# Kernel tuning notes

Measured on AMD Instinct MI355X. Metric: run time of the kernel, lower is better.

The kernel has to match this reference:

```python
import jax, jax.numpy as jnp
import numpy as np

B, T, C, H = 4, 2048, 1024, 16
D = C // H  # head dim = 64

def setup_inputs() -> dict:
    key = jax.random.key(0)
    k1, k2, k3 = jax.random.split(key, 3)
    x = jax.random.normal(k1, (B, T, C), dtype=jnp.float32)
    w_attn = jax.random.normal(k2, (C, 3 * C), dtype=jnp.float32) * 0.02
    b_attn = jnp.zeros((3 * C,), dtype=jnp.float32)
    w_proj = jax.random.normal(k3, (C, C), dtype=jnp.float32) * 0.02
    b_proj = jnp.zeros((C,), dtype=jnp.float32)
    return {"x": x, "w_attn": w_attn, "b_attn": b_attn, "w_proj": w_proj, "b_proj": b_proj}

def reference(x, w_attn, b_attn, w_proj, b_proj):
    Bx, Tx, Cx = x.shape
    qkv = x @ w_attn + b_attn  # [B, T, 3C]
    q, k, v = jnp.split(qkv, 3, axis=2)
    # [B, H, T, D]
    q = q.reshape(Bx, Tx, H, D).swapaxes(1, 2)
    k = k.reshape(Bx, Tx, H, D).swapaxes(1, 2)
    v = v.reshape(Bx, Tx, H, D).swapaxes(1, 2)
    scale = 1.0 / jnp.sqrt(jnp.asarray(D, dtype=x.dtype))
    att = jnp.einsum('bhqd,bhkd->bhqk', q, k) * scale  # [B, H, T, T]
    causal = jnp.tril(jnp.ones((Tx, Tx), dtype=bool))
    att = jnp.where(causal[None, None], att, -jnp.inf)
    att = jax.nn.softmax(att, axis=-1)
    y = jnp.einsum('bhqk,bhkd->bhqd', att, v)  # [B, H, T, D]
    y = y.swapaxes(1, 2).reshape(Bx, Tx, Cx)
    return y @ w_proj + b_proj
```

## Files before the change

### kernel.cpp

```cpp
#include <hip/hip_runtime.h>
#include <hip/hip_bf16.h>
#include <cstdint>

#define B_ 4
#define T_ 2048
#define C_ 1024
#define H_ 16
#define D_ 64

#define BM 128
#define BN 128
#define BK 64
#define NT (C_ / BK)

typedef __bf16 bf16x8 __attribute__((ext_vector_type(8)));
typedef float f32x4 __attribute__((ext_vector_type(4)));

static __device__ __forceinline__ unsigned short f2bf(float f) {
    unsigned int i = __float_as_uint(f);
    unsigned int r = (i + 0x7FFFu + ((i >> 16) & 1u)) >> 16;
    return (unsigned short)r;
}
static __device__ __forceinline__ unsigned short f2bf_hw(float f) {
    __bf16 h = (__bf16)f;
    union { __bf16 h; unsigned short u; } cv;
    cv.h = h;
    return cv.u;
}
static __device__ __forceinline__ float exp2_fast(float x) {
    float r;
    asm("v_exp_f32 %0, %1" : "=v"(r) : "v"(x));
    return r;
}

static __device__ __forceinline__ void gl_lds16(const unsigned short* g,
                                                unsigned short* l) {
    __builtin_amdgcn_global_load_lds(
        (const __attribute__((address_space(1))) unsigned int*)g,
        (__attribute__((address_space(3))) unsigned int*)l, 16, 0, 0);
}

__global__ __launch_bounds__(256)
void convert_f32_bf16(const float* __restrict__ in,
                      unsigned short* __restrict__ out, int n) {
    int i = (blockIdx.x * 256 + threadIdx.x) * 8;
    if (i < n) {
        float4 a = *(const float4*)(in + i);
        float4 b = *(const float4*)(in + i + 4);
        ushort4 s0 = {f2bf(a.x), f2bf(a.y), f2bf(a.z), f2bf(a.w)};
        ushort4 s1 = {f2bf(b.x), f2bf(b.y), f2bf(b.z), f2bf(b.w)};
        *(ushort4*)(out + i) = s0;
        *(ushort4*)(out + i + 4) = s1;
    }
}

__global__ void transpose_f32_bf16(const float* __restrict__ in,
                                   unsigned short* __restrict__ out,
                                   int R, int Cc) {
    __shared__ unsigned short tile[32][33];
    int c0 = blockIdx.x * 32;
    int r0 = blockIdx.y * 32;
    int tx = threadIdx.x, ty = threadIdx.y;
    #pragma unroll
    for (int i = ty; i < 32; i += 8)
        tile[i][tx] = f2bf(in[(size_t)(r0 + i) * Cc + c0 + tx]);
    __syncthreads();
    #pragma unroll
    for (int i = ty; i < 32; i += 8)
        out[(size_t)(c0 + i) * R + r0 + tx] = tile[tx][i];
}

#define GEMM128_CORE(APTR, ASTRIDE, BTPTR)                                    \
    int tid = threadIdx.x;                                                    \
    int nwg = gridDim.x * gridDim.y;                                          \
    int flat = blockIdx.y * gridDim.x + blockIdx.x;                           \
    int swz = (flat & 7) * (nwg >> 3) + (flat >> 3);                          \
    int bx = swz % gridDim.x;                                                 \
    int by = swz / gridDim.x;                                                 \
    int row0 = by * BM;                                                       \
    int col0 = bx * BN;                                                       \
    int wave = tid >> 6, lane = tid & 63;                                     \
    int wm = wave >> 1, wn = wave & 1;                                        \
    int m16 = lane & 15, quad = lane >> 4;                                    \
    int srow = tid >> 3;                                                      \
    int scs = ((tid & 7) ^ (srow & 7)) * 8;                                   \
    const unsigned short* aps = (APTR) + (size_t)(row0 + srow) * (ASTRIDE)    \
                                + scs;                                        \
    const unsigned short* bps = (BTPTR) + (size_t)(col0 + srow) * C_ + scs;   \
    f32x4 acc[4][4];                                                          \
    _Pragma("unroll")                                                         \
    for (int i = 0; i < 4; ++i)                                               \
    _Pragma("unroll")                                                         \
    for (int j = 0; j < 4; ++j)                                               \
        acc[i][j] = (f32x4){0.f, 0.f, 0.f, 0.f};                              \
    auto STAGE = [&](int t, int buf) {                                        \
        int koff = t * BK;                                                    \
        unsigned short* ad = smem + buf * 8192 + tid * 8;                     \
        unsigned short* bd = smem + 16384 + buf * 8192 + tid * 8;             \
        _Pragma("unroll")                                                     \
        for (int l = 0; l < 4; ++l) {                                         \
            gl_lds16(aps + (size_t)(l * 32) * (ASTRIDE) + koff, ad + l * 2048);\
            gl_lds16(bps + (size_t)(l * 32) * C_ + koff, bd + l * 2048);      \
        }                                                                     \
    };                                                                        \
    int rbA = wm * 64 + m16;                                                  \
    int rbB = wn * 64 + m16;                                                  \
    int pc0 = ((0 + quad) ^ (m16 & 7)) * 8;                                   \
    int pc1 = ((4 + quad) ^ (m16 & 7)) * 8;                                   \
    STAGE(0, 0);                                                              \
    asm volatile("s_waitcnt vmcnt(0)" ::: "memory");                          \
    __builtin_amdgcn_s_barrier();                                             \
    for (int t = 0; t < NT; ++t) {                                            \
        int buf = t & 1;                                                      \
        if (t + 1 < NT) STAGE(t + 1, buf ^ 1);                                \
        const unsigned short* Abuf = smem + buf * 8192;                       \
        const unsigned short* Bbuf = smem + 16384 + buf * 8192;               \
        bf16x8 a0[4], a1[4], b0[4], b1[4];                                    \
        _Pragma("unroll")                                                     \
        for (int i = 0; i < 4; ++i) {                                         \
            a0[i] = *(const bf16x8*)(Abuf + (rbA + i * 16) * 64 + pc0);       \
            a1[i] = *(const bf16x8*)(Abuf + (rbA + i * 16) * 64 + pc1);       \
        }                                                                     \
        _Pragma("unroll")                                                     \
        for (int j = 0; j < 4; ++j) {                                         \
            b0[j] = *(const bf16x8*)(Bbuf + (rbB + j * 16) * 64 + pc0);       \
            b1[j] = *(const bf16x8*)(Bbuf + (rbB + j * 16) * 64 + pc1);       \
        }                                                                     \
        __builtin_amdgcn_s_setprio(1);                                        \
        _Pragma("unroll")                                                     \
        for (int i = 0; i < 4; ++i)                                           \
        _Pragma("unroll")                                                     \
        for (int j = 0; j < 4; ++j) {                                         \
            acc[i][j] = __builtin_amdgcn_mfma_f32_16x16x32_bf16(              \
                a0[i], b0[j], acc[i][j], 0, 0, 0);                            \
            acc[i][j] = __builtin_amdgcn_mfma_f32_16x16x32_bf16(              \
                a1[i], b1[j], acc[i][j], 0, 0, 0);                            \
        }                                                                     \
        __builtin_amdgcn_s_setprio(0);                                        \
        asm volatile("s_waitcnt vmcnt(0)" ::: "memory");                      \
        __builtin_amdgcn_s_barrier();                                        \
    }                                                                         \
    __syncthreads();

__global__ __launch_bounds__(256, 2)
void gemm_qkv(const unsigned short* __restrict__ A,
              const unsigned short* __restrict__ Bt,
              const float* __restrict__ bias,
              unsigned short* __restrict__ qkv,
              unsigned short* __restrict__ vt,
              int M, float qscale) {
    __shared__ __align__(16) unsigned short smem[32768];
    GEMM128_CORE(A, C_, Bt)

    float bv[4];
    #pragma unroll
    for (int j = 0; j < 4; ++j)
        bv[j] = bias[col0 + wn * 64 + j * 16 + m16];

    unsigned short* wbuf = smem + wave * 2048;
    bool isV = (col0 >= 2 * C_);
    float sc = (col0 < C_) ? qscale : 1.0f;
    int b_loc = row0 >> 11;
    int trow0 = (row0 & 2047) + wm * 64;
    int head = isV ? ((col0 - 2 * C_ + wn * 64) >> 6) : 0;
    unsigned short* vtb = vt + (size_t)((b_loc * H_ + head) * 64) * T_;

    #pragma unroll
    for (int sub = 0; sub < 4; ++sub) {
        int i0 = (sub >> 1) << 1;
        int j0 = (sub & 1) << 1;
        #pragma unroll
        for (int jj = 0; jj < 2; ++jj) {
            #pragma unroll
            for (int ii = 0; ii < 2; ++ii) {
                #pragma unroll
                for (int rr = 0; rr < 4; ++rr) {
                    int rl = ii * 16 + quad * 4 + rr;
                    int cl = jj * 16 + m16;
                    unsigned short hv =
                        f2bf((acc[i0 + ii][j0 + jj][rr] + bv[j0 + jj]) * sc);
                    if (!isV) wbuf[rl * 40 + cl] = hv;
                    else      wbuf[cl * 40 + rl] = hv;
                }
            }
        }
        __builtin_amdgcn_sched_barrier(0);
        if (!isV) {
            #pragma unroll
            for (int it = 0; it < 4; ++it) {
                int rl = it * 8 + (lane >> 3);
                int cc = (lane & 7) << 2;
                uint2 v2 = *(const uint2*)&wbuf[rl * 40 + cc];
                int rowg = row0 + wm * 64 + i0 * 16 + rl;
                int colg = col0 + wn * 64 + j0 * 16 + cc;
                *(uint2*)&qkv[(size_t)rowg * (2 * C_) + colg] = v2;
            }
        } else {
            #pragma unroll
            for (int it = 0; it < 4; ++it) {
                int dsub = it * 8 + (lane >> 3);
                int tc = (lane & 7) << 2;
                uint2 v2 = *(const uint2*)&wbuf[dsub * 40 + tc];
                int d = j0 * 16 + dsub;
                int tg = trow0 + i0 * 16 + tc;
                *(uint2*)&vtb[(size_t)d * T_ + tg] = v2;
            }
        }
        __builtin_amdgcn_sched_barrier(0);
    }
}

__global__ __launch_bounds__(256, 2)
void gemm_out(const unsigned short* __restrict__ A,
              const unsigned short* __restrict__ Bt,
              const float* __restrict__ bias,
              float* __restrict__ Cmat,
              int M) {
    const int N = C_;
    __shared__ __align__(16) unsigned short smem[32768];
    GEMM128_CORE(A, (2 * C_), Bt)

    #pragma unroll
    for (int j = 0; j < 4; ++j) {
        int col = col0 + wn * 64 + j * 16 + m16;
        float bvv = bias[col];
        #pragma unroll
        for (int i = 0; i < 4; ++i) {
            int row = row0 + wm * 64 + i * 16 + quad * 4;
            #pragma unroll
            for (int rr = 0; rr < 4; ++rr)
                Cmat[(size_t)(row + rr) * N + col] = acc[i][j][rr] + bvv;
        }
    }
}

__global__ __launch_bounds__(256, 4)
void attn_mfma(unsigned short* __restrict__ qkv,
               const unsigned short* __restrict__ vt) {
    __shared__ __align__(16) unsigned short Ks[2][64][64];
    __shared__ __align__(16) unsigned short Vs[2][64][64];
    __shared__ __align__(16) unsigned short Pb[4][16][64];

    int bh = blockIdx.x;
    int b = bh >> 4, h = bh & 15;
    int qb = (T_ / 128 - 1) - blockIdx.y;
    int tid = threadIdx.x;
    int wave = tid >> 6;
    int lane = tid & 63;
    int m16 = lane & 15, quad = lane >> 4;

    const size_t rs = 2 * C_;
    unsigned short* base = qkv + (size_t)b * T_ * rs + h * 64;
    const unsigned short* kb0 = base + C_;
    const unsigned short* vtb = vt + (size_t)bh * 64 * T_;

    bf16x8 qf0[2], qf1[2];
    #pragma unroll
    for (int f = 0; f < 2; ++f) {
        int qrow = qb * 128 + wave * 32 + f * 16 + m16;
        const unsigned short* qp = base + (size_t)qrow * rs;
        qf0[f] = *(const bf16x8*)(qp + quad * 8);
        qf1[f] = *(const bf16x8*)(qp + 32 + quad * 8);
    }

    f32x4 o[2][4];
    #pragma unroll
    for (int f = 0; f < 2; ++f)
        #pragma unroll
        for (int dt = 0; dt < 4; ++dt) o[f][dt] = (f32x4){0.f, 0.f, 0.f, 0.f};
    float lrow[2][4] = {{0.f, 0.f, 0.f, 0.f}, {0.f, 0.f, 0.f, 0.f}};

    int qg0[2];
    qg0[0] = qb * 128 + wave * 32 + quad * 4;
    qg0[1] = qg0[0] + 16;

    int ntiles = 2 * qb + 2;

    int srow = tid >> 3;
    int schs = ((tid & 7) ^ (srow & 7)) * 8;
    const unsigned short* kps = kb0 + (size_t)srow * rs + schs;
    const unsigned short* vps = vtb + (size_t)srow * T_ + schs;
    unsigned short* kdst = &Ks[0][0][0] + wave * 512;
    unsigned short* vdst = &Vs[0][0][0] + wave * 512;

    auto STAGE = [&](int kt, int buf) {
        const unsigned short* ks = kps + (size_t)(kt * 64) * rs;
        const unsigned short* vs = vps + kt * 64;
        unsigned short* kd = kdst + buf * 4096;
        unsigned short* vd = vdst + buf * 4096;
        gl_lds16(ks, kd);
        gl_lds16(ks + (size_t)32 * rs, kd + 2048);
        gl_lds16(vs, vd);
        gl_lds16(vs + (size_t)32 * T_, vd + 2048);
    };

    int kpc0 = ((0 + quad) ^ (m16 & 7)) << 3;
    int kpc1 = ((4 + quad) ^ (m16 & 7)) << 3;

    STAGE(0, 0);
    asm volatile("s_waitcnt vmcnt(0)" ::: "memory");
    __builtin_amdgcn_s_barrier();

    for (int kt = 0; kt < ntiles; ++kt) {
        int cur = kt & 1;
        if (kt + 1 < ntiles) STAGE(kt + 1, cur ^ 1);

        f32x4 s[2][4];
        #pragma unroll
        for (int st = 0; st < 4; ++st) {
            bf16x8 k0 = *(const bf16x8*)&Ks[cur][st * 16 + m16][kpc0];
            bf16x8 k1 = *(const bf16x8*)&Ks[cur][st * 16 + m16][kpc1];
            __builtin_amdgcn_s_setprio(1);
            #pragma unroll
            for (int f = 0; f < 2; ++f) {
                f32x4 a = (f32x4){0.f, 0.f, 0.f, 0.f};
                a = __builtin_amdgcn_mfma_f32_16x16x32_bf16(qf0[f], k0, a, 0, 0, 0);
                a = __builtin_amdgcn_mfma_f32_16x16x32_bf16(qf1[f], k1, a, 0, 0, 0);
                s[f][st] = a;
            }
            __builtin_amdgcn_s_setprio(0);
        }

        if (kt >= 2 * qb) {
            #pragma unroll
            for (int f = 0; f < 2; ++f)
                #pragma unroll
                for (int st = 0; st < 4; ++st) {
                    int kg = kt * 64 + st * 16 + m16;
                    #pragma unroll
                    for (int r = 0; r < 4; ++r)
                        if (kg > qg0[f] + r) s[f][st][r] = -1.0e30f;
                }
        }

        #pragma unroll
        for (int f = 0; f < 2; ++f) {
            #pragma unroll
            for (int st = 0; st < 4; ++st)
                #pragma unroll
                for (int r = 0; r < 4; ++r) {
                    float p = exp2_fast(s[f][st][r]);
                    lrow[f][r] += p;
                    int row = quad * 4 + r;
                    int phys = (st * 2 + (m16 >> 3)) ^ (row & 7);
                    Pb[wave][row][phys * 8 + (m16 & 7)] = f2bf_hw(p);
                }
            __builtin_amdgcn_sched_barrier(0);

            #pragma unroll
            for (int s2 = 0; s2 < 2; ++s2) {
                int pc = ((s2 * 4 + quad) ^ (m16 & 7)) << 3;
                bf16x8 pa = *(const bf16x8*)&Pb[wave][m16][pc];
                __builtin_amdgcn_s_setprio(1);
                #pragma unroll
                for (int dt = 0; dt < 4; ++dt) {
                    bf16x8 vv = *(const bf16x8*)&Vs[cur][dt * 16 + m16][pc];
                    o[f][dt] = __builtin_amdgcn_mfma_f32_16x16x32_bf16(
                        pa, vv, o[f][dt], 0, 0, 0);
                }
                __builtin_amdgcn_s_setprio(0);
            }
            __builtin_amdgcn_sched_barrier(0);
        }

        asm volatile("s_waitcnt vmcnt(0)" ::: "memory");
        __builtin_amdgcn_s_barrier();
    }

    #pragma unroll
    for (int f = 0; f < 2; ++f) {
        float lf[4];
        #pragma unroll
        for (int r = 0; r < 4; ++r) lf[r] = lrow[f][r];
        #pragma unroll
        for (int off = 1; off <= 8; off <<= 1)
            #pragma unroll
            for (int r = 0; r < 4; ++r)
                lf[r] += __shfl_xor(lf[r], off);

        #pragma unroll
        for (int r = 0; r < 4; ++r) {
            float inv = 1.0f / lf[r];
            unsigned short* op = base + (size_t)(qg0[f] + r) * rs;
            #pragma unroll
            for (int dt = 0; dt < 4; ++dt)
                op[dt * 16 + m16] = f2bf_hw(o[f][dt][r] * inv);
        }
    }
}

extern "C" void kernel_launch(void* const* d_in, const int* in_sizes, int n_in,
                              void* d_out, int out_size, void* d_ws, size_t ws_size,
                              hipStream_t stream) {
    const float* x      = (const float*)d_in[0];
    const float* w_attn = (const float*)d_in[1];
    const float* b_attn = (const float*)d_in[2];
    const float* w_proj = (const float*)d_in[3];
    const float* b_proj = (const float*)d_in[4];
    float* out = (float*)d_out;

    unsigned short* ws = (unsigned short*)d_ws;
    unsigned short* xb       = ws;
    unsigned short* w_attn_t = xb + (size_t)B_ * T_ * C_;
    unsigned short* w_proj_t = w_attn_t + (size_t)3 * C_ * C_;
    unsigned short* qkv      = w_proj_t + (size_t)C_ * C_;

    const size_t fixed_hw = (size_t)B_ * T_ * C_ + 4 * (size_t)C_ * C_;
    const size_t per_b_hw = (size_t)T_ * 2 * C_ + (size_t)H_ * 64 * T_;
    int bstep = (ws_size >= (fixed_hw + (size_t)B_ * per_b_hw) * sizeof(unsigned short))
                ? B_ : 1;

    int nx = B_ * T_ * C_;
    convert_f32_bf16<<<nx / 2048, 256, 0, stream>>>(x, xb, nx);
    transpose_f32_bf16<<<dim3(3 * C_ / 32, C_ / 32), dim3(32, 8), 0, stream>>>(
        w_attn, w_attn_t, C_, 3 * C_);
    transpose_f32_bf16<<<dim3(C_ / 32, C_ / 32), dim3(32, 8), 0, stream>>>(
        w_proj, w_proj_t, C_, C_);

    const float QSCALE = 0.125f * 1.44269504088896341f;

    for (int b0 = 0; b0 < B_; b0 += bstep) {
        int M = bstep * T_;
        const unsigned short* xbb = xb + (size_t)b0 * T_ * C_;
        unsigned short* vt = qkv + (size_t)bstep * T_ * 2 * C_;

        gemm_qkv<<<dim3(3 * C_ / BN, M / BM), 256, 0, stream>>>(
            xbb, w_attn_t, b_attn, qkv, vt, M, QSCALE);

        attn_mfma<<<dim3(bstep * H_, T_ / 128), 256, 0, stream>>>(qkv, vt);

        gemm_out<<<dim3(C_ / BN, M / BM), 256, 0, stream>>>(
            qkv, w_proj_t, b_proj, out + (size_t)b0 * T_ * C_, M);
    }
}
```

Measured before the change: 263.2 us.

## Triple-buffer K/V tiles in attention and batch P writes across both row fragments

```diff
diff --git a/kernel.cpp b/kernel.cpp
--- a/kernel.cpp
+++ b/kernel.cpp
@@ -234,12 +234,12 @@
     }
 }
 
-__global__ __launch_bounds__(256, 4)
+__global__ __launch_bounds__(256, 2)
 void attn_mfma(unsigned short* __restrict__ qkv,
                const unsigned short* __restrict__ vt) {
-    __shared__ __align__(16) unsigned short Ks[2][64][64];
-    __shared__ __align__(16) unsigned short Vs[2][64][64];
-    __shared__ __align__(16) unsigned short Pb[4][16][64];
+    __shared__ __align__(16) unsigned short Ks[3][64][64];
+    __shared__ __align__(16) unsigned short Vs[3][64][64];
+    __shared__ __align__(16) unsigned short Pb[4][32][64];
 
     int bh = blockIdx.x;
     int b = bh >> 4, h = bh & 15;
@@ -283,33 +283,36 @@
     unsigned short* kdst = &Ks[0][0][0] + wave * 512;
     unsigned short* vdst = &Vs[0][0][0] + wave * 512;
 
-    auto STAGE = [&](int kt, int buf) {
+    auto STAGE = [&](int kt, int off) {
         const unsigned short* ks = kps + (size_t)(kt * 64) * rs;
         const unsigned short* vs = vps + kt * 64;
-        unsigned short* kd = kdst + buf * 4096;
-        unsigned short* vd = vdst + buf * 4096;
-        gl_lds16(ks, kd);
-        gl_lds16(ks + (size_t)32 * rs, kd + 2048);
-        gl_lds16(vs, vd);
-        gl_lds16(vs + (size_t)32 * T_, vd + 2048);
+        gl_lds16(ks, kdst + off);
+        gl_lds16(ks + (size_t)32 * rs, kdst + off + 2048);
+        gl_lds16(vs, vdst + off);
+        gl_lds16(vs + (size_t)32 * T_, vdst + off + 2048);
     };
 
     int kpc0 = ((0 + quad) ^ (m16 & 7)) << 3;
     int kpc1 = ((4 + quad) ^ (m16 & 7)) << 3;
 
     STAGE(0, 0);
-    asm volatile("s_waitcnt vmcnt(0)" ::: "memory");
+    STAGE(1, 4096);
+    asm volatile("s_waitcnt vmcnt(4)" ::: "memory");
     __builtin_amdgcn_s_barrier();
 
+    int o0 = 0, o1 = 4096, o2 = 8192;
     for (int kt = 0; kt < ntiles; ++kt) {
-        int cur = kt & 1;
-        if (kt + 1 < ntiles) STAGE(kt + 1, cur ^ 1);
+        bool st2 = (kt + 2 < ntiles);
+        if (st2) STAGE(kt + 2, o2);
+
+        const unsigned short* Kc = &Ks[0][0][0] + o0;
+        const unsigned short* Vc = &Vs[0][0][0] + o0;
 
         f32x4 s[2][4];
         #pragma unroll
         for (int st = 0; st < 4; ++st) {
-            bf16x8 k0 = *(const bf16x8*)&Ks[cur][st * 16 + m16][kpc0];
-            bf16x8 k1 = *(const bf16x8*)&Ks[cur][st * 16 + m16][kpc1];
+            bf16x8 k0 = *(const bf16x8*)(Kc + (st * 16 + m16) * 64 + kpc0);
+            bf16x8 k1 = *(const bf16x8*)(Kc + (st * 16 + m16) * 64 + kpc1);
             __builtin_amdgcn_s_setprio(1);
             #pragma unroll
             for (int f = 0; f < 2; ++f) {
@@ -334,37 +337,43 @@
         }
 
         #pragma unroll
-        for (int f = 0; f < 2; ++f) {
+        for (int f = 0; f < 2; ++f)
             #pragma unroll
             for (int st = 0; st < 4; ++st)
                 #pragma unroll
                 for (int r = 0; r < 4; ++r) {
                     float p = exp2_fast(s[f][st][r]);
                     lrow[f][r] += p;
-                    int row = quad * 4 + r;
+                    int row = f * 16 + quad * 4 + r;
                     int phys = (st * 2 + (m16 >> 3)) ^ (row & 7);
                     Pb[wave][row][phys * 8 + (m16 & 7)] = f2bf_hw(p);
                 }
-            __builtin_amdgcn_sched_barrier(0);
-
-            #pragma unroll
-            for (int s2 = 0; s2 < 2; ++s2) {
-                int pc = ((s2 * 4 + quad) ^ (m16 & 7)) << 3;
-                bf16x8 pa = *(const bf16x8*)&Pb[wave][m16][pc];
+        __builtin_amdgcn_sched_barrier(0);
+
+        #pragma unroll
+        for (int s2 = 0; s2 < 2; ++s2) {
+            int pc = ((s2 * 4 + quad) ^ (m16 & 7)) << 3;
+            #pragma unroll
+            for (int f = 0; f < 2; ++f) {
+                bf16x8 pa = *(const bf16x8*)&Pb[wave][f * 16 + m16][pc];
                 __builtin_amdgcn_s_setprio(1);
                 #pragma unroll
                 for (int dt = 0; dt < 4; ++dt) {
-                    bf16x8 vv = *(const bf16x8*)&Vs[cur][dt * 16 + m16][pc];
+                    bf16x8 vv = *(const bf16x8*)(Vc + (dt * 16 + m16) * 64 + pc);
                     o[f][dt] = __builtin_amdgcn_mfma_f32_16x16x32_bf16(
                         pa, vv, o[f][dt], 0, 0, 0);
                 }
                 __builtin_amdgcn_s_setprio(0);
             }
-            __builtin_amdgcn_sched_barrier(0);
-        }
-
-        asm volatile("s_waitcnt vmcnt(0)" ::: "memory");
-        __builtin_amdgcn_s_barrier();
+        }
+        __builtin_amdgcn_sched_barrier(0);
+
+        if (kt + 1 < ntiles) {
+            if (st2) asm volatile("s_waitcnt vmcnt(4)" ::: "memory");
+            else     asm volatile("s_waitcnt vmcnt(0)" ::: "memory");
+            __builtin_amdgcn_s_barrier();
+        }
+        int x = o0; o0 = o1; o1 = o2; o2 = x;
     }
 
     #pragma unroll
```

New measurement: 257.1 us. 2.3% less time.

## Transpose QK^T MFMA so P is written row-contiguous with packed bf16 stores

Applied to the files above, without the earlier changes.

```diff
diff --git a/kernel.cpp b/kernel.cpp
--- a/kernel.cpp
+++ b/kernel.cpp
@@ -30,6 +30,11 @@
 static __device__ __forceinline__ float exp2_fast(float x) {
     float r;
     asm("v_exp_f32 %0, %1" : "=v"(r) : "v"(x));
+    return r;
+}
+static __device__ __forceinline__ unsigned int cvt_pk_bf16(float a, float b) {
+    unsigned int r;
+    asm("v_cvt_pk_bf16_f32 %0, %1, %2" : "=v"(r) : "v"(a), "v"(b));
     return r;
 }
 
@@ -234,12 +239,12 @@
     }
 }
 
-__global__ __launch_bounds__(256, 4)
+__global__ __launch_bounds__(256, 3)
 void attn_mfma(unsigned short* __restrict__ qkv,
                const unsigned short* __restrict__ vt) {
     __shared__ __align__(16) unsigned short Ks[2][64][64];
     __shared__ __align__(16) unsigned short Vs[2][64][64];
-    __shared__ __align__(16) unsigned short Pb[4][16][64];
+    __shared__ __align__(16) unsigned short P2[4][2][16][64];
 
     int bh = blockIdx.x;
     int b = bh >> 4, h = bh & 15;
@@ -268,12 +273,9 @@
     for (int f = 0; f < 2; ++f)
         #pragma unroll
         for (int dt = 0; dt < 4; ++dt) o[f][dt] = (f32x4){0.f, 0.f, 0.f, 0.f};
-    float lrow[2][4] = {{0.f, 0.f, 0.f, 0.f}, {0.f, 0.f, 0.f, 0.f}};
-
-    int qg0[2];
-    qg0[0] = qb * 128 + wave * 32 + quad * 4;
-    qg0[1] = qg0[0] + 16;
-
+    float lrow[2] = {0.f, 0.f};
+
+    int qbase = qb * 128 + wave * 32;
     int ntiles = 2 * qb + 2;
 
     int srow = tid >> 3;
@@ -314,8 +316,8 @@
             #pragma unroll
             for (int f = 0; f < 2; ++f) {
                 f32x4 a = (f32x4){0.f, 0.f, 0.f, 0.f};
-                a = __builtin_amdgcn_mfma_f32_16x16x32_bf16(qf0[f], k0, a, 0, 0, 0);
-                a = __builtin_amdgcn_mfma_f32_16x16x32_bf16(qf1[f], k1, a, 0, 0, 0);
+                a = __builtin_amdgcn_mfma_f32_16x16x32_bf16(k0, qf0[f], a, 0, 0, 0);
+                a = __builtin_amdgcn_mfma_f32_16x16x32_bf16(k1, qf1[f], a, 0, 0, 0);
                 s[f][st] = a;
             }
             __builtin_amdgcn_s_setprio(0);
@@ -323,34 +325,42 @@
 
         if (kt >= 2 * qb) {
             #pragma unroll
-            for (int f = 0; f < 2; ++f)
+            for (int f = 0; f < 2; ++f) {
+                int qg = qbase + f * 16 + m16;
                 #pragma unroll
                 for (int st = 0; st < 4; ++st) {
-                    int kg = kt * 64 + st * 16 + m16;
+                    int kg = kt * 64 + st * 16 + quad * 4;
                     #pragma unroll
                     for (int r = 0; r < 4; ++r)
-                        if (kg > qg0[f] + r) s[f][st][r] = -1.0e30f;
+                        if (kg + r > qg) s[f][st][r] = -1.0e30f;
                 }
-        }
-
-        #pragma unroll
-        for (int f = 0; f < 2; ++f) {
-            #pragma unroll
-            for (int st = 0; st < 4; ++st)
-                #pragma unroll
-                for (int r = 0; r < 4; ++r) {
-                    float p = exp2_fast(s[f][st][r]);
-                    lrow[f][r] += p;
-                    int row = quad * 4 + r;
-                    int phys = (st * 2 + (m16 >> 3)) ^ (row & 7);
-                    Pb[wave][row][phys * 8 + (m16 & 7)] = f2bf_hw(p);
-                }
-            __builtin_amdgcn_sched_barrier(0);
-
-            #pragma unroll
-            for (int s2 = 0; s2 < 2; ++s2) {
-                int pc = ((s2 * 4 + quad) ^ (m16 & 7)) << 3;
-                bf16x8 pa = *(const bf16x8*)&Pb[wave][m16][pc];
+            }
+        }
+
+        #pragma unroll
+        for (int f = 0; f < 2; ++f)
+            #pragma unroll
+            for (int st = 0; st < 4; ++st) {
+                float p0 = exp2_fast(s[f][st][0]);
+                float p1 = exp2_fast(s[f][st][1]);
+                float p2 = exp2_fast(s[f][st][2]);
+                float p3 = exp2_fast(s[f][st][3]);
+                lrow[f] += (p0 + p1) + (p2 + p3);
+                unsigned int d0 = cvt_pk_bf16(p0, p1);
+                unsigned int d1 = cvt_pk_bf16(p2, p3);
+                int pb = (st * 2 + (quad >> 1)) ^ (m16 & 7);
+                int wd = (quad & 1) * 2;
+                *(unsigned int*)&P2[wave][f][m16][pb * 8 + wd * 2]       = d0;
+                *(unsigned int*)&P2[wave][f][m16][pb * 8 + (wd + 1) * 2] = d1;
+            }
+        __builtin_amdgcn_sched_barrier(0);
+
+        #pragma unroll
+        for (int s2 = 0; s2 < 2; ++s2) {
+            int pc = ((s2 * 4 + quad) ^ (m16 & 7)) << 3;
+            #pragma unroll
+            for (int f = 0; f < 2; ++f) {
+                bf16x8 pa = *(const bf16x8*)&P2[wave][f][m16][pc];
                 __builtin_amdgcn_s_setprio(1);
                 #pragma unroll
                 for (int dt = 0; dt < 4; ++dt) {
@@ -360,8 +370,8 @@
                 }
                 __builtin_amdgcn_s_setprio(0);
             }
-            __builtin_amdgcn_sched_barrier(0);
-        }
+        }
+        __builtin_amdgcn_sched_barrier(0);
 
         asm volatile("s_waitcnt vmcnt(0)" ::: "memory");
         __builtin_amdgcn_s_barrier();
@@ -369,22 +379,17 @@
 
     #pragma unroll
     for (int f = 0; f < 2; ++f) {
-        float lf[4];
-        #pragma unroll
-        for (int r = 0; r < 4; ++r) lf[r] = lrow[f][r];
-        #pragma unroll
-        for (int off = 1; off <= 8; off <<= 1)
-            #pragma unroll
-            for (int r = 0; r < 4; ++r)
-                lf[r] += __shfl_xor(lf[r], off);
-
+        float lf = lrow[f];
+        lf += __shfl_xor(lf, 16);
+        lf += __shfl_xor(lf, 32);
+        float inv = 1.0f / lf;
         #pragma unroll
         for (int r = 0; r < 4; ++r) {
-            float inv = 1.0f / lf[r];
-            unsigned short* op = base + (size_t)(qg0[f] + r) * rs;
+            float invr = __shfl(inv, quad * 4 + r);
+            unsigned short* op = base + (size_t)(qbase + f * 16 + quad * 4 + r) * rs;
             #pragma unroll
             for (int dt = 0; dt < 4; ++dt)
-                op[dt * 16 + m16] = f2bf_hw(o[f][dt][r] * inv);
+                op[dt * 16 + m16] = f2bf_hw(o[f][dt][r] * invr);
         }
     }
 }
```

Measured after the change: 245.0 us. -6.9%, faster.
